# Kernel tuning notes

Measured on AMD Instinct MI355X. Metric: run time of the kernel, lower is better.

The kernel has to match this reference:

```python
import jax, jax.numpy as jnp
import numpy as np

T, B, H, N = 1024, 8, 8, 32  # x dim D = H*N*N = 8192


def setup_inputs() -> dict:
    key = jax.random.key(0)
    x = jax.random.normal(key, (T, B, H * N * N), dtype=jnp.float32)
    S = jnp.zeros((B, H, N, N), dtype=jnp.float32)
    scale = jnp.float32(1.0)  # init_scale
    bias = jnp.float32(2.0)   # init_bias
    return {"x": x, "S": S, "scale": scale, "bias": bias}


def reference(x, S, scale, bias):
    Tt, Bb, D = x.shape
    _, Hh, n, _ = S.shape
    xr = x.reshape(Tt, Bb, Hh, n, n)  # [T,B,H,n,n]

    def step(S_c, A):
        # A: [B,H,n,n]
        k = A.mean(axis=-1)            # mean over dim 2 per head -> [B,H,n]
        v = A.mean(axis=-2)            # mean over dim 1 per head -> [B,H,n]
        A_mean = A.mean(axis=(-1, -2))  # [B,H]
        beta = jax.nn.sigmoid(scale * A_mean + bias)  # [B,H]
        k_norm = k / (jnp.linalg.norm(k, axis=-1, keepdims=True) + 1e-6)
        retrieved = jnp.einsum('bhij,bhj->bhi', S_c, k_norm)
        delta = v - retrieved
        outer = delta[..., :, None] * k_norm[..., None, :]  # [B,H,n,n]
        S_new = jnp.tanh(beta[..., None, None] * S_c + outer)
        Sq = jnp.einsum('bhij,bhj->bhi', S_new, k_norm)     # [B,H,n]
        out = Sq * jax.nn.silu(Sq)                          # [B,H,n]
        return S_new, out.reshape(Bb, Hh * n)

    S_final, output = jax.lax.scan(step, S, xr)  # output: [T,B,H*n]
    return output, S_final
```

## Files before the change

### kernel.cpp

```cpp
#include <hip/hip_runtime.h>
#include <math.h>

#define T_STEPS 1024
#define NBH     64
#define NTILE   65536

static __device__ __forceinline__ float fast_rcp(float x) {
  return __builtin_amdgcn_rcpf(x);
}
static __device__ __forceinline__ float fast_sigmoid(float x) {
  return fast_rcp(1.0f + __expf(-x));
}
static __device__ __forceinline__ float fast_tanh2(float y) {
  return 1.0f - 2.0f * fast_rcp(1.0f + __expf(y));
}

template <int CTRL>
static __device__ __forceinline__ float dpp_add(float x) {
  int y = __builtin_amdgcn_update_dpp(0, __float_as_int(x), CTRL, 0xF, 0xF, true);
  return x + __int_as_float(y);
}

static __device__ __forceinline__ float red16(float x) {
  x = dpp_add<0xB1>(x);
  x = dpp_add<0x4E>(x);
  x = dpp_add<0x141>(x);
  x = dpp_add<0x140>(x);
  return x;
}

__global__ __launch_bounds__(256) void stats_kernel(
    const float* __restrict__ x, const float* __restrict__ scale_p,
    const float* __restrict__ bias_p, float* __restrict__ knT2,
    float* __restrict__ vvT2, float* __restrict__ bbT2) {
  const int tid = threadIdx.x;
  const int l   = tid & 63;
  const int m   = l & 7;
  const int g   = l >> 3;
  const int wib = tid >> 6;
  const int job = blockIdx.x * 4 + wib;
  const int bh  = job >> 6;
  const int t0  = (job & 63) << 4;
  const float sc = scale_p[0], bi = bias_p[0];

  __shared__ float kn_s[4][512];
  __shared__ float vv_s[4][512];
  __shared__ float bb_s[4][16];
  float* ks = kn_s[wib];
  float* vs = vv_s[wib];
  float* bs = bb_s[wib];

  const float4* xp = (const float4*)(x + ((size_t)t0 * 64 + bh) * 1024);
  float4 a0 = xp[l], a1 = xp[l + 64], a2 = xp[l + 128], a3 = xp[l + 192];

  for (int tt = 0; tt < 16; ++tt) {
    float4 b0, b1, b2, b3;
    if (tt < 15) {
      const float4* xn = xp + (size_t)(tt + 1) * 16384;
      b0 = xn[l]; b1 = xn[l + 64]; b2 = xn[l + 128]; b3 = xn[l + 192];
    }

    float r0 = (a0.x + a0.y) + (a0.z + a0.w);
    float r1 = (a1.x + a1.y) + (a1.z + a1.w);
    float r2 = (a2.x + a2.y) + (a2.z + a2.w);
    float r3 = (a3.x + a3.y) + (a3.z + a3.w);
    r0 += __shfl_xor(r0, 1); r1 += __shfl_xor(r1, 1);
    r2 += __shfl_xor(r2, 1); r3 += __shfl_xor(r3, 1);
    r0 += __shfl_xor(r0, 2); r1 += __shfl_xor(r1, 2);
    r2 += __shfl_xor(r2, 2); r3 += __shfl_xor(r3, 2);
    r0 += __shfl_xor(r0, 4); r1 += __shfl_xor(r1, 4);
    r2 += __shfl_xor(r2, 4); r3 += __shfl_xor(r3, 4);

    float c0 = a0.x + a1.x + a2.x + a3.x;
    float c1 = a0.y + a1.y + a2.y + a3.y;
    float c2 = a0.z + a1.z + a2.z + a3.z;
    float c3 = a0.w + a1.w + a2.w + a3.w;
    c0 += __shfl_xor(c0, 8);  c1 += __shfl_xor(c1, 8);
    c2 += __shfl_xor(c2, 8);  c3 += __shfl_xor(c3, 8);
    c0 += __shfl_xor(c0, 16); c1 += __shfl_xor(c1, 16);
    c2 += __shfl_xor(c2, 16); c3 += __shfl_xor(c3, 16);
    c0 += __shfl_xor(c0, 32); c1 += __shfl_xor(c1, 32);
    c2 += __shfl_xor(c2, 32); c3 += __shfl_xor(c3, 32);

    float t1 = (r0 + r1) + (r2 + r3);
    float t2 = (r0 * r0 + r1 * r1) + (r2 * r2 + r3 * r3);
    t1 += __shfl_xor(t1, 8);  t2 += __shfl_xor(t2, 8);
    t1 += __shfl_xor(t1, 16); t2 += __shfl_xor(t2, 16);
    t1 += __shfl_xor(t1, 32); t2 += __shfl_xor(t2, 32);
    const float norm = sqrtf(t2) * (1.0f / 32.0f);
    const float kscl = (1.0f / 32.0f) * fast_rcp(norm + 1e-6f);

    if (m == 0) {
      ks[(g)      * 16 + tt] = r0 * kscl;
      ks[(g + 8)  * 16 + tt] = r1 * kscl;
      ks[(g + 16) * 16 + tt] = r2 * kscl;
      ks[(g + 24) * 16 + tt] = r3 * kscl;
    }
    if (l < 8) {
      vs[(4 * m)     * 16 + tt] = c0 * (1.0f / 16.0f);
      vs[(4 * m + 1) * 16 + tt] = c1 * (1.0f / 16.0f);
      vs[(4 * m + 2) * 16 + tt] = c2 * (1.0f / 16.0f);
      vs[(4 * m + 3) * 16 + tt] = c3 * (1.0f / 16.0f);
    }
    if (l == 0) {
      const float mean = t1 * (1.0f / 1024.0f);
      bs[tt] = 2.0f * fast_sigmoid(sc * mean + bi);
    }

    a0 = b0; a1 = b1; a2 = b2; a3 = b3;
  }

  const size_t rowbase = (size_t)bh * 32 * T_STEPS + t0;
#pragma unroll
  for (int rep = 0; rep < 2; ++rep) {
    const int c = l + rep * 64;
    const int e = c >> 2;
    const int q = c & 3;
    const float4 kv = *(const float4*)&ks[e * 16 + q * 4];
    const float4 vv = *(const float4*)&vs[e * 16 + q * 4];
    *(float4*)(knT2 + rowbase + (size_t)e * T_STEPS + q * 4) = kv;
    *(float4*)(vvT2 + rowbase + (size_t)e * T_STEPS + q * 4) = vv;
  }
  if (l < 4) {
    const float4 bv = *(const float4*)&bs[l * 4];
    *(float4*)(bbT2 + (size_t)bh * T_STEPS + t0 + l * 4) = bv;
  }
}

__global__ __launch_bounds__(256, 1) void scan_kernel(
    const float* __restrict__ S0, const float* __restrict__ knT2,
    const float* __restrict__ vvT2, const float* __restrict__ bbT2,
    float* __restrict__ out, float* __restrict__ Sfin) {
  const int tid  = threadIdx.x;
  const int lane = tid & 63;
  const int g    = lane >> 4;
  const int s    = lane & 15;
  const int w    = blockIdx.x * 4 + (tid >> 6);
  const int bh   = w >> 3;
  const int i    = (w & 7) * 4 + g;
  const int chain = bh * 32 + i;

  const float2 sini = *(const float2*)(S0 + (size_t)bh * 1024 + i * 32 + 2 * s);
  float Sa = sini.x, Sb = sini.y;

  const float* kn0p = knT2 + ((size_t)bh * 32 + 2 * s) * T_STEPS;
  const float* kn1p = kn0p + T_STEPS;
  const float* vp   = vvT2 + ((size_t)bh * 32 + i) * T_STEPS;
  const float* bp   = bbT2 + (size_t)bh * T_STEPS;

  float Ak0[16], Ak1[16], Av[16], Ab[16];
  float Bk0[16], Bk1[16], Bv[16], Bb[16];

#define LOAD_BLK(K0, K1, VV, BE, TOFF)                                    \
  do {                                                                    \
    const int _to = (TOFF);                                               \
    _Pragma("unroll")                                                     \
    for (int qq = 0; qq < 4; ++qq) {                                      \
      *(float4*)&K0[4 * qq] = *(const float4*)(kn0p + _to + 4 * qq);      \
      *(float4*)&K1[4 * qq] = *(const float4*)(kn1p + _to + 4 * qq);      \
      *(float4*)&VV[4 * qq] = *(const float4*)(vp   + _to + 4 * qq);      \
      *(float4*)&BE[4 * qq] = *(const float4*)(bp   + _to + 4 * qq);      \
    }                                                                     \
  } while (0)

#define STEP_BLK(K0, K1, VV, BE, TBASE)                                   \
  do {                                                                    \
    float oacc = 0.0f;                                                    \
    _Pragma("unroll")                                                     \
    for (int u = 0; u < 16; ++u) {                                        \
      const float c0 = K0[u], c1 = K1[u];                                 \
      const float r  = red16(Sa * c0 + Sb * c1);                          \
      const float D2 = fmaf(-2.0f, r, VV[u]);              \
      const float B2 = BE[u];                                             \
      Sa = fast_tanh2(fmaf(B2, Sa, D2 * c0));                             \
      Sb = fast_tanh2(fmaf(B2, Sb, D2 * c1));                             \
      const float qv = red16(Sa * c0 + Sb * c1);                          \
      const float o  = qv * qv * fast_sigmoid(qv);                        \
      oacc = (u == s) ? o : oacc;                                         \
    }                                                                     \
    outp[(size_t)((TBASE) + s) * 2048] = oacc;                            \
  } while (0)

  float* outp = out + chain;

  LOAD_BLK(Ak0, Ak1, Av, Ab, 0);

  for (int t0 = 0; t0 < T_STEPS; t0 += 32) {
    const int tB = t0 + 16;
    const int tA2 = (t0 + 32 < T_STEPS) ? t0 + 32 : t0;
    LOAD_BLK(Bk0, Bk1, Bv, Bb, tB);
    STEP_BLK(Ak0, Ak1, Av, Ab, t0);
    LOAD_BLK(Ak0, Ak1, Av, Ab, tA2);
    STEP_BLK(Bk0, Bk1, Bv, Bb, tB);
  }

#undef LOAD_BLK
#undef STEP_BLK

  float2 sfin; sfin.x = Sa; sfin.y = Sb;
  *(float2*)(Sfin + (size_t)bh * 1024 + i * 32 + 2 * s) = sfin;
}

extern "C" void kernel_launch(void* const* d_in, const int* in_sizes, int n_in,
                              void* d_out, int out_size, void* d_ws, size_t ws_size,
                              hipStream_t stream) {
  const float* x     = (const float*)d_in[0];
  const float* S0    = (const float*)d_in[1];
  const float* scale = (const float*)d_in[2];
  const float* bias  = (const float*)d_in[3];
  float* out = (float*)d_out;

  float* knT2 = (float*)d_ws;
  float* vvT2 = knT2 + (size_t)NTILE * 32;
  float* bbT2 = vvT2 + (size_t)NTILE * 32;

  stats_kernel<<<1024, 256, 0, stream>>>(x, scale, bias, knT2, vvT2, bbT2);

  float* Sfin = out + (size_t)T_STEPS * 2048;
  scan_kernel<<<128, 256, 0, stream>>>(S0, knT2, vvT2, bbT2, out, Sfin);
}
```

Baseline: 465.0 us.

## Fuse stats and scan kernels with per-chunk flags for producer-consumer overlap

Merges the stats pass and the sequential scan into one launch. The first 128 blocks run the scan and the remaining blocks produce per-(head, time-chunk) records, each published with a release fence and a flag. Scan blocks spin on these flags, with sleep and a bounded spin count, before loading each chunk. The stats work is ordered chunk-major so early time chunks finish first. This overlaps reading x with the serial recurrence and stores records as contiguous chunks. The cost is a flag-init kernel, spin-wait overhead, and reliance on scan blocks being scheduled alongside producers without deadlock. The bounded spin can silently continue on stale data if that assumption fails.

After: 764.8 us. 64.5% more time.

```diff
diff --git a/kernel.cpp b/kernel.cpp
--- a/kernel.cpp
+++ b/kernel.cpp
@@ -1,9 +1,14 @@
 #include <hip/hip_runtime.h>
 #include <math.h>
 
-#define T_STEPS 1024
-#define NBH     64
-#define NTILE   65536
+#define T_STEPS     1024
+#define NBH         64
+#define NCHUNK      64
+#define NREC        (NBH * NCHUNK)
+#define REC_F       1088
+#define SCAN_BLOCKS 128
+#define STATS_BLOCKS 1024
+#define SPIN_BOUND  (1 << 20)
 
 static __device__ __forceinline__ float fast_rcp(float x) {
   return __builtin_amdgcn_rcpf(x);
@@ -29,109 +34,115 @@
   return x;
 }
 
-__global__ __launch_bounds__(256) void stats_kernel(
-    const float* __restrict__ x, const float* __restrict__ scale_p,
-    const float* __restrict__ bias_p, float* __restrict__ knT2,
-    float* __restrict__ vvT2, float* __restrict__ bbT2) {
+__global__ __launch_bounds__(256) void init_flags(int* __restrict__ flags) {
+  const int gid = blockIdx.x * 256 + threadIdx.x;
+  if (gid < NREC) flags[gid] = 0;
+}
+
+__global__ __launch_bounds__(256, 1) void fused_kernel(
+    const float* __restrict__ x, const float* __restrict__ S0,
+    const float* __restrict__ scale_p, const float* __restrict__ bias_p,
+    float* __restrict__ recs, int* __restrict__ flags,
+    float* __restrict__ out, float* __restrict__ Sfin) {
   const int tid = threadIdx.x;
-  const int l   = tid & 63;
-  const int m   = l & 7;
-  const int g   = l >> 3;
-  const int wib = tid >> 6;
-  const int job = blockIdx.x * 4 + wib;
-  const int bh  = job >> 6;
-  const int t0  = (job & 63) << 4;
-  const float sc = scale_p[0], bi = bias_p[0];
-
-  __shared__ float kn_s[4][512];
-  __shared__ float vv_s[4][512];
-  __shared__ float bb_s[4][16];
-  float* ks = kn_s[wib];
-  float* vs = vv_s[wib];
-  float* bs = bb_s[wib];
-
-  const float4* xp = (const float4*)(x + ((size_t)t0 * 64 + bh) * 1024);
-  float4 a0 = xp[l], a1 = xp[l + 64], a2 = xp[l + 128], a3 = xp[l + 192];
-
-  for (int tt = 0; tt < 16; ++tt) {
-    float4 b0, b1, b2, b3;
-    if (tt < 15) {
-      const float4* xn = xp + (size_t)(tt + 1) * 16384;
-      b0 = xn[l]; b1 = xn[l + 64]; b2 = xn[l + 128]; b3 = xn[l + 192];
+
+  if (blockIdx.x >= SCAN_BLOCKS) {
+    const int l   = tid & 63;
+    const int m   = l & 7;
+    const int g   = l >> 3;
+    const int wib = tid >> 6;
+    const int job = (blockIdx.x - SCAN_BLOCKS) * 4 + wib;
+    const int bh  = job & 63;
+    const int ch  = job >> 6;
+    const float sc = scale_p[0], bi = bias_p[0];
+
+    __shared__ float kn_s[4][512];
+    __shared__ float vv_s[4][512];
+    __shared__ float bb_s[4][16];
+    float* ks = kn_s[wib];
+    float* vs = vv_s[wib];
+    float* bs = bb_s[wib];
+
+    const float4* xp = (const float4*)(x + (((size_t)ch * 16) * 64 + bh) * 1024);
+    float4 a0 = xp[l], a1 = xp[l + 64], a2 = xp[l + 128], a3 = xp[l + 192];
+    const float4* x1 = xp + 16384;
+    float4 b0 = x1[l], b1 = x1[l + 64], b2 = x1[l + 128], b3 = x1[l + 192];
+
+#pragma unroll
+    for (int tt = 0; tt < 16; ++tt) {
+      float4 n0 = a0, n1 = a1, n2 = a2, n3 = a3;
+      if (tt < 14) {
+        const float4* xn = xp + (size_t)(tt + 2) * 16384;
+        n0 = xn[l]; n1 = xn[l + 64]; n2 = xn[l + 128]; n3 = xn[l + 192];
+      }
+
+      float r0 = (a0.x + a0.y) + (a0.z + a0.w);
+      float r1 = (a1.x + a1.y) + (a1.z + a1.w);
+      float r2 = (a2.x + a2.y) + (a2.z + a2.w);
+      float r3 = (a3.x + a3.y) + (a3.z + a3.w);
+      r0 += __shfl_xor(r0, 1); r1 += __shfl_xor(r1, 1);
+      r2 += __shfl_xor(r2, 1); r3 += __shfl_xor(r3, 1);
+      r0 += __shfl_xor(r0, 2); r1 += __shfl_xor(r1, 2);
+      r2 += __shfl_xor(r2, 2); r3 += __shfl_xor(r3, 2);
+      r0 += __shfl_xor(r0, 4); r1 += __shfl_xor(r1, 4);
+      r2 += __shfl_xor(r2, 4); r3 += __shfl_xor(r3, 4);
+
+      float c0 = a0.x + a1.x + a2.x + a3.x;
+      float c1 = a0.y + a1.y + a2.y + a3.y;
+      float c2 = a0.z + a1.z + a2.z + a3.z;
+      float c3 = a0.w + a1.w + a2.w + a3.w;
+      c0 += __shfl_xor(c0, 8);  c1 += __shfl_xor(c1, 8);
+      c2 += __shfl_xor(c2, 8);  c3 += __shfl_xor(c3, 8);
+      c0 += __shfl_xor(c0, 16); c1 += __shfl_xor(c1, 16);
+      c2 += __shfl_xor(c2, 16); c3 += __shfl_xor(c3, 16);
+      c0 += __shfl_xor(c0, 32); c1 += __shfl_xor(c1, 32);
+      c2 += __shfl_xor(c2, 32); c3 += __shfl_xor(c3, 32);
+
+      float t1 = (r0 + r1) + (r2 + r3);
+      float t2 = (r0 * r0 + r1 * r1) + (r2 * r2 + r3 * r3);
+      t1 += __shfl_xor(t1, 8);  t2 += __shfl_xor(t2, 8);
+      t1 += __shfl_xor(t1, 16); t2 += __shfl_xor(t2, 16);
+      t1 += __shfl_xor(t1, 32); t2 += __shfl_xor(t2, 32);
+      const float norm = sqrtf(t2) * (1.0f / 32.0f);
+      const float kscl = (1.0f / 32.0f) * fast_rcp(norm + 1e-6f);
+
+      if (m == 0) {
+        ks[(g)      * 16 + tt] = r0 * kscl;
+        ks[(g + 8)  * 16 + tt] = r1 * kscl;
+        ks[(g + 16) * 16 + tt] = r2 * kscl;
+        ks[(g + 24) * 16 + tt] = r3 * kscl;
+      }
+      if (l < 8) {
+        vs[(4 * m)     * 16 + tt] = c0 * (1.0f / 16.0f);
+        vs[(4 * m + 1) * 16 + tt] = c1 * (1.0f / 16.0f);
+        vs[(4 * m + 2) * 16 + tt] = c2 * (1.0f / 16.0f);
+        vs[(4 * m + 3) * 16 + tt] = c3 * (1.0f / 16.0f);
+      }
+      if (l == 0) {
+        const float mean = t1 * (1.0f / 1024.0f);
+        bs[tt] = 2.0f * fast_sigmoid(sc * mean + bi);
+      }
+
+      a0 = b0; a1 = b1; a2 = b2; a3 = b3;
+      b0 = n0; b1 = n1; b2 = n2; b3 = n3;
     }
 
-    float r0 = (a0.x + a0.y) + (a0.z + a0.w);
-    float r1 = (a1.x + a1.y) + (a1.z + a1.w);
-    float r2 = (a2.x + a2.y) + (a2.z + a2.w);
-    float r3 = (a3.x + a3.y) + (a3.z + a3.w);
-    r0 += __shfl_xor(r0, 1); r1 += __shfl_xor(r1, 1);
-    r2 += __shfl_xor(r2, 1); r3 += __shfl_xor(r3, 1);
-    r0 += __shfl_xor(r0, 2); r1 += __shfl_xor(r1, 2);
-    r2 += __shfl_xor(r2, 2); r3 += __shfl_xor(r3, 2);
-    r0 += __shfl_xor(r0, 4); r1 += __shfl_xor(r1, 4);
-    r2 += __shfl_xor(r2, 4); r3 += __shfl_xor(r3, 4);
-
-    float c0 = a0.x + a1.x + a2.x + a3.x;
-    float c1 = a0.y + a1.y + a2.y + a3.y;
-    float c2 = a0.z + a1.z + a2.z + a3.z;
-    float c3 = a0.w + a1.w + a2.w + a3.w;
-    c0 += __shfl_xor(c0, 8);  c1 += __shfl_xor(c1, 8);
-    c2 += __shfl_xor(c2, 8);  c3 += __shfl_xor(c3, 8);
-    c0 += __shfl_xor(c0, 16); c1 += __shfl_xor(c1, 16);
-    c2 += __shfl_xor(c2, 16); c3 += __shfl_xor(c3, 16);
-    c0 += __shfl_xor(c0, 32); c1 += __shfl_xor(c1, 32);
-    c2 += __shfl_xor(c2, 32); c3 += __shfl_xor(c3, 32);
-
-    float t1 = (r0 + r1) + (r2 + r3);
-    float t2 = (r0 * r0 + r1 * r1) + (r2 * r2 + r3 * r3);
-    t1 += __shfl_xor(t1, 8);  t2 += __shfl_xor(t2, 8);
-    t1 += __shfl_xor(t1, 16); t2 += __shfl_xor(t2, 16);
-    t1 += __shfl_xor(t1, 32); t2 += __shfl_xor(t2, 32);
-    const float norm = sqrtf(t2) * (1.0f / 32.0f);
-    const float kscl = (1.0f / 32.0f) * fast_rcp(norm + 1e-6f);
-
-    if (m == 0) {
-      ks[(g)      * 16 + tt] = r0 * kscl;
-      ks[(g + 8)  * 16 + tt] = r1 * kscl;
-      ks[(g + 16) * 16 + tt] = r2 * kscl;
-      ks[(g + 24) * 16 + tt] = r3 * kscl;
+    float* rec = recs + ((size_t)bh * NCHUNK + ch) * REC_F;
+#pragma unroll
+    for (int rep = 0; rep < 2; ++rep) {
+      const int cc = l + rep * 64;
+      *(float4*)(rec + 4 * cc)       = *(const float4*)&ks[4 * cc];
+      *(float4*)(rec + 512 + 4 * cc) = *(const float4*)&vs[4 * cc];
     }
-    if (l < 8) {
-      vs[(4 * m)     * 16 + tt] = c0 * (1.0f / 16.0f);
-      vs[(4 * m + 1) * 16 + tt] = c1 * (1.0f / 16.0f);
-      vs[(4 * m + 2) * 16 + tt] = c2 * (1.0f / 16.0f);
-      vs[(4 * m + 3) * 16 + tt] = c3 * (1.0f / 16.0f);
-    }
-    if (l == 0) {
-      const float mean = t1 * (1.0f / 1024.0f);
-      bs[tt] = 2.0f * fast_sigmoid(sc * mean + bi);
-    }
-
-    a0 = b0; a1 = b1; a2 = b2; a3 = b3;
+    if (l < 4) *(float4*)(rec + 1024 + 4 * l) = *(const float4*)&bs[4 * l];
+
+    __builtin_amdgcn_fence(__ATOMIC_RELEASE, "agent");
+    if (l == 0)
+      __hip_atomic_store(&flags[bh * NCHUNK + ch], 1, __ATOMIC_RELAXED,
+                         __HIP_MEMORY_SCOPE_AGENT);
+    return;
   }
 
-  const size_t rowbase = (size_t)bh * 32 * T_STEPS + t0;
-#pragma unroll
-  for (int rep = 0; rep < 2; ++rep) {
-    const int c = l + rep * 64;
-    const int e = c >> 2;
-    const int q = c & 3;
-    const float4 kv = *(const float4*)&ks[e * 16 + q * 4];
-    const float4 vv = *(const float4*)&vs[e * 16 + q * 4];
-    *(float4*)(knT2 + rowbase + (size_t)e * T_STEPS + q * 4) = kv;
-    *(float4*)(vvT2 + rowbase + (size_t)e * T_STEPS + q * 4) = vv;
-  }
-  if (l < 4) {
-    const float4 bv = *(const float4*)&bs[l * 4];
-    *(float4*)(bbT2 + (size_t)bh * T_STEPS + t0 + l * 4) = bv;
-  }
-}
-
-__global__ __launch_bounds__(256, 1) void scan_kernel(
-    const float* __restrict__ S0, const float* __restrict__ knT2,
-    const float* __restrict__ vvT2, const float* __restrict__ bbT2,
-    float* __restrict__ out, float* __restrict__ Sfin) {
-  const int tid  = threadIdx.x;
   const int lane = tid & 63;
   const int g    = lane >> 4;
   const int s    = lane & 15;
@@ -143,23 +154,41 @@
   const float2 sini = *(const float2*)(S0 + (size_t)bh * 1024 + i * 32 + 2 * s);
   float Sa = sini.x, Sb = sini.y;
 
-  const float* kn0p = knT2 + ((size_t)bh * 32 + 2 * s) * T_STEPS;
-  const float* kn1p = kn0p + T_STEPS;
-  const float* vp   = vvT2 + ((size_t)bh * 32 + i) * T_STEPS;
-  const float* bp   = bbT2 + (size_t)bh * T_STEPS;
+  const float* recb = recs + (size_t)bh * NCHUNK * REC_F;
+  const int*   flg  = flags + bh * NCHUNK;
+  float* outp = out + chain;
 
   float Ak0[16], Ak1[16], Av[16], Ab[16];
   float Bk0[16], Bk1[16], Bv[16], Bb[16];
 
-#define LOAD_BLK(K0, K1, VV, BE, TOFF)                                    \
+#define FLAG_LD(c) \
+  __hip_atomic_load(&flg[(c)], __ATOMIC_RELAXED, __HIP_MEMORY_SCOPE_AGENT)
+
+#define WAITCHUNK(fv, c)                                                  \
   do {                                                                    \
-    const int _to = (TOFF);                                               \
+    int _f = (fv);                                                        \
+    int _n = 0;                                                           \
+    while (_f == 0 && _n < SPIN_BOUND) {                                  \
+      __builtin_amdgcn_s_sleep(2);                                        \
+      _f = FLAG_LD(c);                                                    \
+      ++_n;                                                               \
+    }                                                                     \
+    __builtin_amdgcn_fence(__ATOMIC_ACQUIRE, "agent");                    \
+  } while (0)
+
+#define LOAD_REC(K0, K1, VV, BE, CHK)                                     \
+  do {                                                                    \
+    const float* _r  = recb + (size_t)(CHK) * REC_F;                      \
+    const float* _k0 = _r + (2 * s) * 16;                                 \
+    const float* _k1 = _r + (2 * s + 1) * 16;                             \
+    const float* _v  = _r + 512 + i * 16;                                 \
+    const float* _b  = _r + 1024;                                         \
     _Pragma("unroll")                                                     \
     for (int qq = 0; qq < 4; ++qq) {                                      \
-      *(float4*)&K0[4 * qq] = *(const float4*)(kn0p + _to + 4 * qq);      \
-      *(float4*)&K1[4 * qq] = *(const float4*)(kn1p + _to + 4 * qq);      \
-      *(float4*)&VV[4 * qq] = *(const float4*)(vp   + _to + 4 * qq);      \
-      *(float4*)&BE[4 * qq] = *(const float4*)(bp   + _to + 4 * qq);      \
+      *(float4*)&K0[4 * qq] = *(const float4*)(_k0 + 4 * qq);             \
+      *(float4*)&K1[4 * qq] = *(const float4*)(_k1 + 4 * qq);             \
+      *(float4*)&VV[4 * qq] = *(const float4*)(_v  + 4 * qq);             \
+      *(float4*)&BE[4 * qq] = *(const float4*)(_b  + 4 * qq);             \
     }                                                                     \
   } while (0)
 
@@ -181,21 +210,28 @@
     outp[(size_t)((TBASE) + s) * 2048] = oacc;                            \
   } while (0)
 
-  float* outp = out + chain;
-
-  LOAD_BLK(Ak0, Ak1, Av, Ab, 0);
-
-  for (int t0 = 0; t0 < T_STEPS; t0 += 32) {
-    const int tB = t0 + 16;
-    const int tA2 = (t0 + 32 < T_STEPS) ? t0 + 32 : t0;
-    LOAD_BLK(Bk0, Bk1, Bv, Bb, tB);
-    STEP_BLK(Ak0, Ak1, Av, Ab, t0);
-    LOAD_BLK(Ak0, Ak1, Av, Ab, tA2);
-    STEP_BLK(Bk0, Bk1, Bv, Bb, tB);
+  int f0 = FLAG_LD(0);
+  WAITCHUNK(f0, 0);
+  LOAD_REC(Ak0, Ak1, Av, Ab, 0);
+  int fB = FLAG_LD(1);
+
+  for (int c0 = 0; c0 < NCHUNK; c0 += 2) {
+    const int cB  = c0 + 1;
+    const int cA2 = (c0 + 2 < NCHUNK) ? c0 + 2 : c0;
+    WAITCHUNK(fB, cB);
+    LOAD_REC(Bk0, Bk1, Bv, Bb, cB);
+    int fA = FLAG_LD(cA2);
+    STEP_BLK(Ak0, Ak1, Av, Ab, c0 * 16);
+    WAITCHUNK(fA, cA2);
+    LOAD_REC(Ak0, Ak1, Av, Ab, cA2);
+    fB = FLAG_LD((cB + 2 < NCHUNK) ? cB + 2 : cB);
+    STEP_BLK(Bk0, Bk1, Bv, Bb, cB * 16);
   }
 
-#undef LOAD_BLK
 #undef STEP_BLK
+#undef LOAD_REC
+#undef WAITCHUNK
+#undef FLAG_LD
 
   float2 sfin; sfin.x = Sa; sfin.y = Sb;
   *(float2*)(Sfin + (size_t)bh * 1024 + i * 32 + 2 * s) = sfin;
@@ -210,12 +246,12 @@
   const float* bias  = (const float*)d_in[3];
   float* out = (float*)d_out;
 
-  float* knT2 = (float*)d_ws;
-  float* vvT2 = knT2 + (size_t)NTILE * 32;
-  float* bbT2 = vvT2 + (size_t)NTILE * 32;
-
-  stats_kernel<<<1024, 256, 0, stream>>>(x, scale, bias, knT2, vvT2, bbT2);
+  float* recs = (float*)d_ws;
+  int* flags  = (int*)(recs + (size_t)NREC * REC_F);
+
+  init_flags<<<16, 256, 0, stream>>>(flags);
 
   float* Sfin = out + (size_t)T_STEPS * 2048;
-  scan_kernel<<<128, 256, 0, stream>>>(S0, knT2, vvT2, bbT2, out, Sfin);
-}
+  fused_kernel<<<SCAN_BLOCKS + STATS_BLOCKS, 256, 0, stream>>>(
+      x, S0, scale, bias, recs, flags, out, Sfin);
+}
```

## Process two state rows per 16-lane group in scan, deepen stats prefetch

Applied to the files above, without the earlier changes.

The scan kernel now has each 16-lane group carry two rows of the state matrix instead of one. This halves the block count to 64 and interleaves two independent recurrence chains per lane, giving more instruction-level parallelism to hide the latency of the DPP reductions and transcendental ops. The shared key and beta loads are reused across both rows, and the outputs are written as float2 pairs. The stats kernel also prefetches x two timesteps ahead instead of one. The trade-off is fewer workgroups (less spread across CUs) and more registers per thread.

Result: slower. 529.1 us (+13.8%).

```diff
diff --git a/kernel.cpp b/kernel.cpp
--- a/kernel.cpp
+++ b/kernel.cpp
@@ -52,12 +52,14 @@
 
   const float4* xp = (const float4*)(x + ((size_t)t0 * 64 + bh) * 1024);
   float4 a0 = xp[l], a1 = xp[l + 64], a2 = xp[l + 128], a3 = xp[l + 192];
+  const float4* xq = xp + 16384;
+  float4 b0 = xq[l], b1 = xq[l + 64], b2 = xq[l + 128], b3 = xq[l + 192];
 
   for (int tt = 0; tt < 16; ++tt) {
-    float4 b0, b1, b2, b3;
-    if (tt < 15) {
-      const float4* xn = xp + (size_t)(tt + 1) * 16384;
-      b0 = xn[l]; b1 = xn[l + 64]; b2 = xn[l + 128]; b3 = xn[l + 192];
+    float4 n0 = a0, n1 = a1, n2 = a2, n3 = a3;
+    if (tt < 14) {
+      const float4* xn = xp + (size_t)(tt + 2) * 16384;
+      n0 = xn[l]; n1 = xn[l + 64]; n2 = xn[l + 128]; n3 = xn[l + 192];
     }
 
     float r0 = (a0.x + a0.y) + (a0.z + a0.w);
@@ -108,6 +110,7 @@
     }
 
     a0 = b0; a1 = b1; a2 = b2; a3 = b3;
+    b0 = n0; b1 = n1; b2 = n2; b3 = n3;
   }
 
   const size_t rowbase = (size_t)bh * 32 * T_STEPS + t0;
@@ -136,69 +139,84 @@
   const int g    = lane >> 4;
   const int s    = lane & 15;
   const int w    = blockIdx.x * 4 + (tid >> 6);
-  const int bh   = w >> 3;
-  const int i    = (w & 7) * 4 + g;
-  const int chain = bh * 32 + i;
-
-  const float2 sini = *(const float2*)(S0 + (size_t)bh * 1024 + i * 32 + 2 * s);
-  float Sa = sini.x, Sb = sini.y;
+  const int bh   = w >> 2;
+  const int ww   = w & 3;
+  const int i1   = ww * 8 + g * 2;
+  const int chain = bh * 32 + i1;
+
+  const float2 si1 = *(const float2*)(S0 + (size_t)bh * 1024 + i1 * 32 + 2 * s);
+  const float2 si2 = *(const float2*)(S0 + (size_t)bh * 1024 + (i1 + 1) * 32 + 2 * s);
+  float S1a = si1.x, S1b = si1.y;
+  float S2a = si2.x, S2b = si2.y;
 
   const float* kn0p = knT2 + ((size_t)bh * 32 + 2 * s) * T_STEPS;
   const float* kn1p = kn0p + T_STEPS;
-  const float* vp   = vvT2 + ((size_t)bh * 32 + i) * T_STEPS;
+  const float* vp1  = vvT2 + ((size_t)bh * 32 + i1) * T_STEPS;
+  const float* vp2  = vp1 + T_STEPS;
   const float* bp   = bbT2 + (size_t)bh * T_STEPS;
 
-  float Ak0[16], Ak1[16], Av[16], Ab[16];
-  float Bk0[16], Bk1[16], Bv[16], Bb[16];
-
-#define LOAD_BLK(K0, K1, VV, BE, TOFF)                                    \
+  float Ak0[16], Ak1[16], Av1[16], Av2[16], Ab[16];
+  float Bk0[16], Bk1[16], Bv1[16], Bv2[16], Bb[16];
+
+#define LOAD_BLK(K0, K1, V1, V2, BE, TOFF)                                \
   do {                                                                    \
     const int _to = (TOFF);                                               \
     _Pragma("unroll")                                                     \
     for (int qq = 0; qq < 4; ++qq) {                                      \
       *(float4*)&K0[4 * qq] = *(const float4*)(kn0p + _to + 4 * qq);      \
       *(float4*)&K1[4 * qq] = *(const float4*)(kn1p + _to + 4 * qq);      \
-      *(float4*)&VV[4 * qq] = *(const float4*)(vp   + _to + 4 * qq);      \
+      *(float4*)&V1[4 * qq] = *(const float4*)(vp1  + _to + 4 * qq);      \
+      *(float4*)&V2[4 * qq] = *(const float4*)(vp2  + _to + 4 * qq);      \
       *(float4*)&BE[4 * qq] = *(const float4*)(bp   + _to + 4 * qq);      \
     }                                                                     \
   } while (0)
 
-#define STEP_BLK(K0, K1, VV, BE, TBASE)                                   \
+#define STEP_BLK(K0, K1, V1, V2, BE, TBASE)                               \
   do {                                                                    \
-    float oacc = 0.0f;                                                    \
+    float oacc1 = 0.0f, oacc2 = 0.0f;                                     \
     _Pragma("unroll")                                                     \
     for (int u = 0; u < 16; ++u) {                                        \
       const float c0 = K0[u], c1 = K1[u];                                 \
-      const float r  = red16(Sa * c0 + Sb * c1);                          \
-      const float D2 = fmaf(-2.0f, r, VV[u]);              \
       const float B2 = BE[u];                                             \
-      Sa = fast_tanh2(fmaf(B2, Sa, D2 * c0));                             \
-      Sb = fast_tanh2(fmaf(B2, Sb, D2 * c1));                             \
-      const float qv = red16(Sa * c0 + Sb * c1);                          \
-      const float o  = qv * qv * fast_sigmoid(qv);                        \
-      oacc = (u == s) ? o : oacc;                                         \
+      const float r1 = red16(S1a * c0 + S1b * c1);                        \
+      const float r2 = red16(S2a * c0 + S2b * c1);                        \
+      const float D1 = fmaf(-2.0f, r1, V1[u]);             \
+      const float D2 = fmaf(-2.0f, r2, V2[u]);                            \
+      S1a = fast_tanh2(fmaf(B2, S1a, D1 * c0));                           \
+      S1b = fast_tanh2(fmaf(B2, S1b, D1 * c1));                           \
+      S2a = fast_tanh2(fmaf(B2, S2a, D2 * c0));                           \
+      S2b = fast_tanh2(fmaf(B2, S2b, D2 * c1));                           \
+      const float q1 = red16(S1a * c0 + S1b * c1);                        \
+      const float q2 = red16(S2a * c0 + S2b * c1);                        \
+      const float o1 = q1 * q1 * fast_sigmoid(q1);                        \
+      const float o2 = q2 * q2 * fast_sigmoid(q2);                        \
+      oacc1 = (u == s) ? o1 : oacc1;                                      \
+      oacc2 = (u == s) ? o2 : oacc2;                                      \
     }                                                                     \
-    outp[(size_t)((TBASE) + s) * 2048] = oacc;                            \
+    float2 ov; ov.x = oacc1; ov.y = oacc2;                                \
+    *(float2*)(outp + (size_t)((TBASE) + s) * 2048) = ov;                 \
   } while (0)
 
   float* outp = out + chain;
 
-  LOAD_BLK(Ak0, Ak1, Av, Ab, 0);
+  LOAD_BLK(Ak0, Ak1, Av1, Av2, Ab, 0);
 
   for (int t0 = 0; t0 < T_STEPS; t0 += 32) {
     const int tB = t0 + 16;
     const int tA2 = (t0 + 32 < T_STEPS) ? t0 + 32 : t0;
-    LOAD_BLK(Bk0, Bk1, Bv, Bb, tB);
-    STEP_BLK(Ak0, Ak1, Av, Ab, t0);
-    LOAD_BLK(Ak0, Ak1, Av, Ab, tA2);
-    STEP_BLK(Bk0, Bk1, Bv, Bb, tB);
+    LOAD_BLK(Bk0, Bk1, Bv1, Bv2, Bb, tB);
+    STEP_BLK(Ak0, Ak1, Av1, Av2, Ab, t0);
+    LOAD_BLK(Ak0, Ak1, Av1, Av2, Ab, tA2);
+    STEP_BLK(Bk0, Bk1, Bv1, Bv2, Bb, tB);
   }
 
 #undef LOAD_BLK
 #undef STEP_BLK
 
-  float2 sfin; sfin.x = Sa; sfin.y = Sb;
-  *(float2*)(Sfin + (size_t)bh * 1024 + i * 32 + 2 * s) = sfin;
+  float2 f1; f1.x = S1a; f1.y = S1b;
+  float2 f2; f2.x = S2a; f2.y = S2b;
+  *(float2*)(Sfin + (size_t)bh * 1024 + i1 * 32 + 2 * s) = f1;
+  *(float2*)(Sfin + (size_t)bh * 1024 + (i1 + 1) * 32 + 2 * s) = f2;
 }
 
 extern "C" void kernel_launch(void* const* d_in, const int* in_sizes, int n_in,
@@ -217,5 +235,5 @@
   stats_kernel<<<1024, 256, 0, stream>>>(x, scale, bias, knT2, vvT2, bbT2);
 
   float* Sfin = out + (size_t)T_STEPS * 2048;
-  scan_kernel<<<128, 256, 0, stream>>>(S0, knT2, vvT2, bbT2, out, Sfin);
-}
+  scan_kernel<<<64, 256, 0, stream>>>(S0, knT2, vvT2, bbT2, out, Sfin);
+}
```
